# Performance work log

Measured on AMD Instinct MI355X. Metric: run time of the kernel, lower is better.

The kernel has to match this reference:

```python
import jax, jax.numpy as jnp
import numpy as np

D_MODEL = 1024
N_HEADS = 16
D_K = D_MODEL // N_HEADS
THETA = 10000.0
MAX_SEQ = 2048


def _trunc_normal(key, shape, std):
    # approximate trunc_normal in [-3std, 3std] via clipping (init only; values irrelevant to math)
    return jnp.clip(jax.random.normal(key, shape) * std, -3 * std, 3 * std).astype(jnp.float32)


def setup_inputs() -> dict:
    key = jax.random.key(0)
    kx, kq, kk, kv, ko = jax.random.split(key, 5)
    std = np.sqrt(2.0 / (D_MODEL + D_MODEL))
    x = jax.random.normal(kx, (2, 2048, D_MODEL), dtype=jnp.float32)
    W_q = _trunc_normal(kq, (D_MODEL, D_MODEL), std)
    W_k = _trunc_normal(kk, (D_MODEL, D_MODEL), std)
    W_v = _trunc_normal(kv, (D_MODEL, D_MODEL), std)
    W_o = _trunc_normal(ko, (D_MODEL, D_MODEL), std)
    return {"x": x, "W_q": W_q, "W_k": W_k, "W_v": W_v, "W_o": W_o}


def _rope(x, positions):
    # x: [b, n, s, d_k]; interleaved even/odd pairing: (x0,x1),(x2,x3),...
    d = x.shape[-1]
    inv_freq = THETA ** (-2.0 * jnp.arange(0, d // 2, dtype=jnp.float32) / d)
    angles = positions.astype(jnp.float32)[:, None] * inv_freq[None, :]  # [s, d/2]
    cos, sin = jnp.cos(angles), jnp.sin(angles)
    xp = x.reshape(x.shape[:-1] + (d // 2, 2))
    x_even, x_odd = xp[..., 0], xp[..., 1]
    out_even = x_even * cos - x_odd * sin
    out_odd = x_even * sin + x_odd * cos
    return jnp.stack((out_even, out_odd), axis=-1).reshape(x.shape)


def reference(x, W_q, W_k, W_v, W_o):
    b, s, _ = x.shape
    def split_heads(t):
        return t.reshape(b, s, N_HEADS, D_K).transpose(0, 2, 1, 3)  # b n s d
    Q = split_heads(x @ W_q.T)
    K = split_heads(x @ W_k.T)
    V = split_heads(x @ W_v.T)
    pos = jnp.arange(s)
    Q = _rope(Q, pos)
    K = _rope(K, pos)
    score = jnp.einsum('bnqd,bnkd->bnqk', Q, K) / jnp.sqrt(jnp.float32(D_K))
    causal = jnp.triu(jnp.ones((s, s), dtype=bool), k=1)
    score = jnp.where(causal[None, None], -jnp.inf, score)
    attn = jax.nn.softmax(score, axis=-1)
    out = jnp.einsum('bnqk,bnkd->bnqd', attn, V)
    out = out.transpose(0, 2, 1, 3).reshape(b, s, D_MODEL)
    return out @ W_o.T
```

## Files before the change

### kernel.cpp

```cpp
#include <hip/hip_runtime.h>

typedef float f32x4 __attribute__((ext_vector_type(4)));
typedef __bf16 bf16x8 __attribute__((ext_vector_type(8)));

#define D_MODEL 1024
#define SEQ     2048
#define NB      2
#define NH      16
#define DK      64

__device__ __forceinline__ unsigned short f2bf(float f) {
    union { float f; unsigned int u; } un; un.f = f;
    unsigned int r = un.u + 0x7fffu + ((un.u >> 16) & 1u);
    return (unsigned short)(r >> 16);
}

__device__ __forceinline__ unsigned cvtpk(float lo, float hi) {
    unsigned r;
    asm("v_cvt_pk_bf16_f32 %0, %1, %2" : "=v"(r) : "v"(lo), "v"(hi));
    return r;
}

__device__ __forceinline__ void gload16(const void* g, void* l) {
    __builtin_amdgcn_global_load_lds((__attribute__((address_space(1))) void*)g,
                                     (__attribute__((address_space(3))) void*)l,
                                     16, 0, 0);
}

__global__ __launch_bounds__(256) void cast5(
    const float* __restrict__ x,  const float* __restrict__ wq,
    const float* __restrict__ wk, const float* __restrict__ wv,
    const float* __restrict__ wo,
    unsigned short* __restrict__ xb,  unsigned short* __restrict__ wqb,
    unsigned short* __restrict__ wkb, unsigned short* __restrict__ wvb,
    unsigned short* __restrict__ wob, float2* __restrict__ tab)
{
    if (blockIdx.y == 5) {
        int idx = blockIdx.x * 256 + threadIdx.x;
        if (idx < SEQ * 32) {
            int ss = idx >> 5, p = idx & 31;
            float freq = exp2f(-0.41524101186f * (float)p);
            float sn, cs;
            sincosf((float)ss * freq, &sn, &cs);
            tab[idx] = make_float2(cs, sn);
        }
        return;
    }
    const float* src; unsigned short* dst; int n8;
    switch (blockIdx.y) {
        case 0:  src = x;  dst = xb;  n8 = (NB*SEQ*D_MODEL)/8; break;
        case 1:  src = wq; dst = wqb; n8 = (D_MODEL*D_MODEL)/8; break;
        case 2:  src = wk; dst = wkb; n8 = (D_MODEL*D_MODEL)/8; break;
        case 3:  src = wv; dst = wvb; n8 = (D_MODEL*D_MODEL)/8; break;
        default: src = wo; dst = wob; n8 = (D_MODEL*D_MODEL)/8; break;
    }
    int stride = gridDim.x * blockDim.x;
    for (int i = blockIdx.x * blockDim.x + threadIdx.x; i < n8; i += stride) {
        const float4* p = (const float4*)src + (size_t)i * 2;
        float4 a = p[0], b = p[1];
        union { unsigned short h[8]; uint4 v; } u;
        u.h[0] = f2bf(a.x); u.h[1] = f2bf(a.y); u.h[2] = f2bf(a.z); u.h[3] = f2bf(a.w);
        u.h[4] = f2bf(b.x); u.h[5] = f2bf(b.y); u.h[6] = f2bf(b.z); u.h[7] = f2bf(b.w);
        ((uint4*)dst)[i] = u.v;
    }
}

template <int MODE>
__global__ __launch_bounds__(256) void gemm_bt(
    const unsigned short* __restrict__ A,
    const unsigned short* __restrict__ B0,
    const unsigned short* __restrict__ B1,
    const unsigned short* __restrict__ B2,
    float* __restrict__ outF,
    unsigned short* __restrict__ Qh,
    unsigned short* __restrict__ Kh,
    unsigned short* __restrict__ Vt,
    const float2* __restrict__ tab,
    int M, int K)
{
    __shared__ __align__(16) unsigned short SM[3][2][128 * 32];

    const int lane = threadIdx.x & 63;
    const int wid  = threadIdx.x >> 6;
    const int l15 = lane & 15, lhi = lane >> 4;
    const int m0 = blockIdx.y * 128;
    const int n0 = blockIdx.x * 128;
    const int z  = (MODE == 1) ? (int)blockIdx.z : 0;
    const unsigned short* B = (z == 0) ? B0 : (z == 1) ? B1 : B2;
    const int waveM = (wid >> 1) * 64;
    const int waveN = (wid & 1) * 64;

    f32x4 acc[4][4];
    f32x4 zero = {0.f, 0.f, 0.f, 0.f};
#pragma unroll
    for (int m = 0; m < 4; ++m)
#pragma unroll
        for (int n = 0; n < 4; ++n) acc[m][n] = zero;

    const int lrow = lane >> 2;
    const int lcol = (lane & 3) * 8;

    auto STAGE = [&](int buf, int k0) {
#pragma unroll
        for (int q = 0; q < 2; ++q) {
            int rbase = wid * 32 + q * 16;
            gload16(A + (size_t)(m0 + rbase + lrow) * K + k0 + lcol,
                    (char*)&SM[buf][0][0] + rbase * 64);
            gload16(B + (size_t)(n0 + rbase + lrow) * K + k0 + lcol,
                    (char*)&SM[buf][1][0] + rbase * 64);
        }
    };

    const int NK = K >> 5;
    STAGE(0, 0);
    STAGE(1, 32);

    for (int k = 0; k < NK; ++k) {
        if (k < NK - 1) asm volatile("s_waitcnt vmcnt(4)" ::: "memory");
        else            asm volatile("s_waitcnt vmcnt(0)" ::: "memory");
        __builtin_amdgcn_s_barrier();
        __builtin_amdgcn_sched_barrier(0);
        if (k + 2 < NK) STAGE((k + 2) % 3, (k + 2) << 5);

        const unsigned short* as = SM[k % 3][0];
        const unsigned short* bs = SM[k % 3][1];
        bf16x8 af[4], bfr[4];
#pragma unroll
        for (int m = 0; m < 4; ++m)
            af[m] = *(const bf16x8*)(as + (waveM + m * 16 + l15) * 32 + lhi * 8);
#pragma unroll
        for (int n = 0; n < 4; ++n)
            bfr[n] = *(const bf16x8*)(bs + (waveN + n * 16 + l15) * 32 + lhi * 8);
        __builtin_amdgcn_s_setprio(1);
#pragma unroll
        for (int m = 0; m < 4; ++m)
#pragma unroll
            for (int n = 0; n < 4; ++n)
                acc[m][n] = __builtin_amdgcn_mfma_f32_16x16x32_bf16(af[m], bfr[n], acc[m][n], 0, 0, 0);
        __builtin_amdgcn_s_setprio(0);
    }

    if constexpr (MODE == 0) {
#pragma unroll
        for (int n = 0; n < 4; ++n) {
            int col = n0 + waveN + n * 16 + l15;
#pragma unroll
            for (int m = 0; m < 4; ++m) {
                int rowb = m0 + waveM + m * 16 + (lhi << 2);
#pragma unroll
                for (int r = 0; r < 4; ++r)
                    outF[(size_t)(rowb + r) * D_MODEL + col] = acc[m][n][r];
            }
        }
    } else {
        __syncthreads();
        unsigned short* Ct = ((unsigned short*)SM) + wid * 4608;
        const int colg0 = n0 + waveN;
        const int hh    = (colg0 >> 6) & (NH - 1);
        const int rowg0 = m0 + waveM;
        const int bb    = rowg0 >> 11;
        const size_t bhh = (size_t)(bb * NH + hh);

#pragma unroll
        for (int n = 0; n < 4; ++n) {
            int cl = n * 16 + l15;
#pragma unroll
            for (int m = 0; m < 4; ++m) {
#pragma unroll
                for (int r = 0; r < 4; ++r) {
                    float v  = acc[m][n][r];
                    float pv = __shfl_xor(v, 1);
                    int rl = m * 16 + (lhi << 2) + r;
                    if (z == 2) {
                        Ct[cl * 72 + rl] = f2bf(v);
                    } else {
                        int ss = (rowg0 + rl) & (SEQ - 1);
                        float2 cs = tab[(ss << 5) + (cl >> 1)];
                        float o = (cl & 1) ? (pv * cs.y + v * cs.x)
                                           : (v * cs.x - pv * cs.y);
                        if (z == 0) o *= 0.18033688011f;
                        Ct[rl * 72 + cl] = f2bf(o);
                    }
                }
            }
        }
        asm volatile("s_waitcnt lgkmcnt(0)" ::: "memory");

        const int lr = lane >> 3;
        const int lc = (lane & 7) << 3;
#pragma unroll
        for (int i = 0; i < 8; ++i) {
            int rl = i * 8 + lr;
            uint4 w = *(const uint4*)&Ct[rl * 72 + lc];
            if (z == 2) {
                int ss0 = rowg0 & (SEQ - 1);
                *(uint4*)(Vt + (bhh * DK + rl) * SEQ + ss0 + lc) = w;
            } else {
                int ss = (rowg0 + rl) & (SEQ - 1);
                unsigned short* dst = (z == 0) ? Qh : Kh;
                *(uint4*)(dst + (bhh * SEQ + ss) * DK + lc) = w;
            }
        }
    }
}

__global__ __launch_bounds__(256) void attn_kernel(
    const unsigned short* __restrict__ Qh,
    const unsigned short* __restrict__ Kh,
    const unsigned short* __restrict__ Vt,
    unsigned short* __restrict__ O)
{
    __shared__ unsigned short Ks[2][64 * 64];
    __shared__ unsigned short Vs[2][64 * 64];
    __shared__ unsigned short P[4][16 * 64];

    const int tid  = threadIdx.x;
    const int lane = tid & 63;
    const int wid  = tid >> 6;
    const int l15 = lane & 15, lhi = lane >> 4;
    const int bh = blockIdx.x;
    const int pi = blockIdx.y;
    const int b = bh >> 4, h = bh & 15;

    const unsigned short* Qb = Qh + (size_t)bh * SEQ * DK;
    const unsigned short* Kb = Kh + (size_t)bh * SEQ * DK;
    const unsigned short* Vb = Vt + (size_t)bh * DK * SEQ;

    auto STAGE = [&](int buf, int kv0s) {
#pragma unroll
        for (int c = 0; c < 2; ++c) {
            int ub = c * 256 + wid * 64;
            int u  = ub + lane;
            int kr = u >> 3;
            int kc = (u & 7) ^ (kr & 7);
            gload16(Kb + (size_t)(kv0s + kr) * DK + kc * 8, &Ks[buf][(size_t)ub * 8]);
        }
#pragma unroll
        for (int c = 0; c < 2; ++c) {
            int ub = c * 256 + wid * 64;
            int u  = ub + lane;
            int vr = u >> 3;
            int vc = (u & 7) ^ (vr & 7);
            gload16(Vb + (size_t)vr * SEQ + kv0s + vc * 8, &Vs[buf][(size_t)ub * 8]);
        }
    };

    const f32x4 zero = {0.f, 0.f, 0.f, 0.f};
    const f32x4 ninf = {-1e30f, -1e30f, -1e30f, -1e30f};

    STAGE(0, 0);
    int cur = 0;

    for (int ph = 0; ph < 2; ++ph) {
        const int qt = ph ? (31 - pi) : pi;
        const int ktl = qt;
        const int q0 = qt * 64;
        const int qw = q0 + wid * 16;

        bf16x8 qf[2];
#pragma unroll
        for (int kk = 0; kk < 2; ++kk)
            qf[kk] = *(const bf16x8*)(Qb + (size_t)(qw + l15) * DK + kk * 32 + lhi * 8);

        f32x4 oacc[4];
#pragma unroll
        for (int nd = 0; nd < 4; ++nd) oacc[nd] = zero;
        float mrow = -1e30f;
        float lrow = 0.f;

        for (int kt = 0; kt <= ktl; ++kt) {
            const int kv0 = kt << 6;
            const bool diag = (kt == ktl);
            const int nlim = diag ? (wid + 1) : 4;

            asm volatile("s_waitcnt vmcnt(0)" ::: "memory");
            __builtin_amdgcn_s_barrier();
            __builtin_amdgcn_sched_barrier(0);

            const bool hasNext = (kt < ktl) || (ph == 0);
            if (hasNext) STAGE(cur ^ 1, (kt < ktl) ? (kv0 + 64) : 0);

            f32x4 s[4];
#pragma unroll
            for (int n = 0; n < 4; ++n) s[n] = (n < nlim) ? zero : ninf;

            const int sw = l15 & 7;
            __builtin_amdgcn_s_setprio(1);
#pragma unroll
            for (int n = 0; n < 4; ++n) {
                if (n < nlim) {
                    int r = n * 16 + l15;
                    bf16x8 k0 = *(const bf16x8*)&Ks[cur][r * 64 + ((lhi ^ sw) << 3)];
                    bf16x8 k1 = *(const bf16x8*)&Ks[cur][r * 64 + (((4 + lhi) ^ sw) << 3)];
                    s[n] = __builtin_amdgcn_mfma_f32_16x16x32_bf16(k0, qf[0], s[n], 0, 0, 0);
                    s[n] = __builtin_amdgcn_mfma_f32_16x16x32_bf16(k1, qf[1], s[n], 0, 0, 0);
                }
            }
            __builtin_amdgcn_s_setprio(0);

            if (diag) {
                const int qg = qw + l15;
#pragma unroll
                for (int n = 0; n < 4; ++n) {
                    if (n < nlim) {
#pragma unroll
                        for (int r = 0; r < 4; ++r) {
                            int kg = kv0 + n * 16 + (lhi << 2) + r;
                            if (kg > qg) s[n][r] = -1e30f;
                        }
                    }
                }
            }

            float mx = fmaxf(fmaxf(s[0][0], s[0][1]), fmaxf(s[0][2], s[0][3]));
#pragma unroll
            for (int n = 1; n < 4; ++n)
                mx = fmaxf(mx, fmaxf(fmaxf(s[n][0], s[n][1]), fmaxf(s[n][2], s[n][3])));
            mx = fmaxf(mx, __shfl_xor(mx, 16));
            mx = fmaxf(mx, __shfl_xor(mx, 32));

            float alpha = 1.f;
            const int allDefer = __all(mx <= mrow + 8.f);
            if (!allDefer) {
                float mn = fmaxf(mrow, mx);
                alpha = __builtin_amdgcn_exp2f(mrow - mn);
                mrow = mn;
            }

#pragma unroll
            for (int n = 0; n < 4; ++n)
#pragma unroll
                for (int r = 0; r < 4; ++r)
                    s[n][r] = __builtin_amdgcn_exp2f(s[n][r] - mrow);

            float rs = 0.f;
#pragma unroll
            for (int n = 0; n < 4; ++n)
                rs += (s[n][0] + s[n][1]) + (s[n][2] + s[n][3]);
            rs += __shfl_xor(rs, 16);
            rs += __shfl_xor(rs, 32);
            lrow = allDefer ? (lrow + rs) : (lrow * alpha + rs);

#pragma unroll
            for (int n = 0; n < 4; ++n) {
                uint2 pk;
                pk.x = cvtpk(s[n][0], s[n][1]);
                pk.y = cvtpk(s[n][2], s[n][3]);
                int cW = 2 * n + (lhi >> 1);
                *(uint2*)&P[wid][(l15 << 6) + ((cW ^ sw) << 3) + ((lhi & 1) << 2)] = pk;
            }

            if (!allDefer) {
                float a0 = __shfl(alpha, (lhi << 2) + 0);
                float a1 = __shfl(alpha, (lhi << 2) + 1);
                float a2 = __shfl(alpha, (lhi << 2) + 2);
                float a3 = __shfl(alpha, (lhi << 2) + 3);
#pragma unroll
                for (int nd = 0; nd < 4; ++nd) {
                    oacc[nd][0] *= a0; oacc[nd][1] *= a1;
                    oacc[nd][2] *= a2; oacc[nd][3] *= a3;
                }
            }

            asm volatile("s_waitcnt lgkmcnt(0)" ::: "memory");
            const int kklim = diag ? ((nlim + 1) >> 1) : 2;
            bf16x8 pa[2];
#pragma unroll
            for (int kk = 0; kk < 2; ++kk)
                if (kk < kklim)
                    pa[kk] = *(const bf16x8*)&P[wid][(l15 << 6) + ((((kk << 2) + lhi) ^ sw) << 3)];

            __builtin_amdgcn_s_setprio(1);
#pragma unroll
            for (int nd = 0; nd < 4; ++nd)
#pragma unroll
                for (int kk = 0; kk < 2; ++kk)
                    if (kk < kklim) {
                        int rd = nd * 16 + l15;
                        bf16x8 vf = *(const bf16x8*)&Vs[cur][rd * 64 + ((((kk << 2) + lhi) ^ sw) << 3)];
                        oacc[nd] = __builtin_amdgcn_mfma_f32_16x16x32_bf16(pa[kk], vf, oacc[nd], 0, 0, 0);
                    }
            __builtin_amdgcn_s_setprio(0);

            cur ^= 1;
        }

        float inv = 1.f / lrow;
        float i0 = __shfl(inv, (lhi << 2) + 0);
        float i1 = __shfl(inv, (lhi << 2) + 1);
        float i2 = __shfl(inv, (lhi << 2) + 2);
        float i3 = __shfl(inv, (lhi << 2) + 3);
#pragma unroll
        for (int nd = 0; nd < 4; ++nd) {
            int d = nd * 16 + l15;
            int rowb = qw + (lhi << 2);
            O[((size_t)(b * SEQ + rowb + 0)) * D_MODEL + h * DK + d] = f2bf(oacc[nd][0] * i0);
            O[((size_t)(b * SEQ + rowb + 1)) * D_MODEL + h * DK + d] = f2bf(oacc[nd][1] * i1);
            O[((size_t)(b * SEQ + rowb + 2)) * D_MODEL + h * DK + d] = f2bf(oacc[nd][2] * i2);
            O[((size_t)(b * SEQ + rowb + 3)) * D_MODEL + h * DK + d] = f2bf(oacc[nd][3] * i3);
        }
    }
}

extern "C" void kernel_launch(void* const* d_in, const int* in_sizes, int n_in,
                              void* d_out, int out_size, void* d_ws, size_t ws_size,
                              hipStream_t stream)
{
    const float* x  = (const float*)d_in[0];
    const float* Wq = (const float*)d_in[1];
    const float* Wk = (const float*)d_in[2];
    const float* Wv = (const float*)d_in[3];
    const float* Wo = (const float*)d_in[4];
    float* out = (float*)d_out;

    char* ws = (char*)d_ws;
    unsigned short* xb  = (unsigned short*)(ws);
    unsigned short* Wqb = (unsigned short*)(ws + ( 8ull << 20));
    unsigned short* Wkb = (unsigned short*)(ws + (10ull << 20));
    unsigned short* Wvb = (unsigned short*)(ws + (12ull << 20));
    unsigned short* Wob = (unsigned short*)(ws + (14ull << 20));
    unsigned short* Qh  = (unsigned short*)(ws + (16ull << 20));
    unsigned short* Kh  = (unsigned short*)(ws + (24ull << 20));
    unsigned short* Vt  = (unsigned short*)(ws + (32ull << 20));
    float2*         tab = (float2*)(ws + (40ull << 20));
    unsigned short* attn = xb;

    cast5<<<dim3(512, 6), 256, 0, stream>>>(x, Wq, Wk, Wv, Wo, xb, Wqb, Wkb, Wvb, Wob, tab);

    gemm_bt<1><<<dim3(D_MODEL / 128, (NB * SEQ) / 128, 3), 256, 0, stream>>>(
        xb, Wqb, Wkb, Wvb, nullptr, Qh, Kh, Vt, tab, NB * SEQ, D_MODEL);

    attn_kernel<<<dim3(NB * NH, 16), 256, 0, stream>>>(Qh, Kh, Vt, attn);

    gemm_bt<0><<<dim3(D_MODEL / 128, (NB * SEQ) / 128, 1), 256, 0, stream>>>(
        attn, Wob, Wob, Wob, out, nullptr, nullptr, nullptr, nullptr, NB * SEQ, D_MODEL);
}
```

Measured before the change: 118.9 us.

## Remap GEMM and attention blocks for XCD locality; one q-tile per attention block

The GEMMs now launch a 1-D grid whose block index is remapped so that consecutive blocks on the same XCD share A/B tiles, and the output projection uses 64x128 tiles so it launches more blocks. The attention kernel drops the paired short/long q-tile scheme and launches one block per (head, q-tile), mapping heads to XCDs and serpentining q-tiles for load balance and L2 reuse of K/V. The aim is better L2 hit rates and occupancy. The cost is uneven per-block work in attention, which now depends on the hardware scheduler to balance it.

```diff
diff --git a/kernel.cpp b/kernel.cpp
--- a/kernel.cpp
+++ b/kernel.cpp
@@ -65,7 +65,7 @@
     }
 }
 
-template <int MODE>
+template <int MODE, int BM, int BN>
 __global__ __launch_bounds__(256) void gemm_bt(
     const unsigned short* __restrict__ A,
     const unsigned short* __restrict__ B0,
@@ -78,36 +78,53 @@
     const float2* __restrict__ tab,
     int M, int K)
 {
-    __shared__ __align__(16) unsigned short SM[3][2][128 * 32];
+    constexpr int PER_STAGE = (BM + BN) / 64;
+    constexpr int WM = BM / 2, WN = BN / 2;
+    constexpr int FM = WM / 16, FN = WN / 16;
+    __shared__ __align__(16) unsigned short SM[3 * (BM + BN) * 32];
 
     const int lane = threadIdx.x & 63;
     const int wid  = threadIdx.x >> 6;
     const int l15 = lane & 15, lhi = lane >> 4;
-    const int m0 = blockIdx.y * 128;
-    const int n0 = blockIdx.x * 128;
-    const int z  = (MODE == 1) ? (int)blockIdx.z : 0;
+
+    const int L  = blockIdx.x;
+    const int yl = L & 7;
+    const int t  = L >> 3;
+    const int bx = t & 7;
+    const int t2 = t >> 3;
+    int y, z;
+    if constexpr (MODE == 1) { y = ((t2 & 3) << 3) | yl; z = t2 >> 2; }
+    else                     { y = (t2 << 3) | yl;       z = 0;       }
+    const int m0 = y * BM;
+    const int n0 = bx * BN;
     const unsigned short* B = (z == 0) ? B0 : (z == 1) ? B1 : B2;
-    const int waveM = (wid >> 1) * 64;
-    const int waveN = (wid & 1) * 64;
-
-    f32x4 acc[4][4];
+    const int waveM = (wid >> 1) * WM;
+    const int waveN = (wid & 1) * WN;
+
+    f32x4 acc[FM][FN];
     f32x4 zero = {0.f, 0.f, 0.f, 0.f};
 #pragma unroll
-    for (int m = 0; m < 4; ++m)
-#pragma unroll
-        for (int n = 0; n < 4; ++n) acc[m][n] = zero;
+    for (int m = 0; m < FM; ++m)
+#pragma unroll
+        for (int n = 0; n < FN; ++n) acc[m][n] = zero;
 
     const int lrow = lane >> 2;
     const int lcol = (lane & 3) * 8;
 
     auto STAGE = [&](int buf, int k0) {
-#pragma unroll
-        for (int q = 0; q < 2; ++q) {
-            int rbase = wid * 32 + q * 16;
+        unsigned short* as = SM + buf * (BM + BN) * 32;
+        unsigned short* bs = as + BM * 32;
+#pragma unroll
+        for (int q = 0; q < BM / 64; ++q) {
+            int rbase = wid * (BM / 4) + q * 16;
             gload16(A + (size_t)(m0 + rbase + lrow) * K + k0 + lcol,
-                    (char*)&SM[buf][0][0] + rbase * 64);
+                    (char*)as + rbase * 64);
+        }
+#pragma unroll
+        for (int q = 0; q < BN / 64; ++q) {
+            int rbase = wid * (BN / 4) + q * 16;
             gload16(B + (size_t)(n0 + rbase + lrow) * K + k0 + lcol,
-                    (char*)&SM[buf][1][0] + rbase * 64);
+                    (char*)bs + rbase * 64);
         }
     };
 
@@ -116,36 +133,40 @@
     STAGE(1, 32);
 
     for (int k = 0; k < NK; ++k) {
-        if (k < NK - 1) asm volatile("s_waitcnt vmcnt(4)" ::: "memory");
-        else            asm volatile("s_waitcnt vmcnt(0)" ::: "memory");
+        if (k < NK - 1) {
+            if constexpr (PER_STAGE == 4) asm volatile("s_waitcnt vmcnt(4)" ::: "memory");
+            else                          asm volatile("s_waitcnt vmcnt(3)" ::: "memory");
+        } else {
+            asm volatile("s_waitcnt vmcnt(0)" ::: "memory");
+        }
         __builtin_amdgcn_s_barrier();
         __builtin_amdgcn_sched_barrier(0);
         if (k + 2 < NK) STAGE((k + 2) % 3, (k + 2) << 5);
 
-        const unsigned short* as = SM[k % 3][0];
-        const unsigned short* bs = SM[k % 3][1];
-        bf16x8 af[4], bfr[4];
-#pragma unroll
-        for (int m = 0; m < 4; ++m)
+        const unsigned short* as = SM + (k % 3) * (BM + BN) * 32;
+        const unsigned short* bs = as + BM * 32;
+        bf16x8 af[FM], bfr[FN];
+#pragma unroll
+        for (int m = 0; m < FM; ++m)
             af[m] = *(const bf16x8*)(as + (waveM + m * 16 + l15) * 32 + lhi * 8);
 #pragma unroll
-        for (int n = 0; n < 4; ++n)
+        for (int n = 0; n < FN; ++n)
             bfr[n] = *(const bf16x8*)(bs + (waveN + n * 16 + l15) * 32 + lhi * 8);
         __builtin_amdgcn_s_setprio(1);
 #pragma unroll
-        for (int m = 0; m < 4; ++m)
-#pragma unroll
-            for (int n = 0; n < 4; ++n)
+        for (int m = 0; m < FM; ++m)
+#pragma unroll
+            for (int n = 0; n < FN; ++n)
                 acc[m][n] = __builtin_amdgcn_mfma_f32_16x16x32_bf16(af[m], bfr[n], acc[m][n], 0, 0, 0);
         __builtin_amdgcn_s_setprio(0);
     }
 
     if constexpr (MODE == 0) {
 #pragma unroll
-        for (int n = 0; n < 4; ++n) {
+        for (int n = 0; n < FN; ++n) {
             int col = n0 + waveN + n * 16 + l15;
 #pragma unroll
-            for (int m = 0; m < 4; ++m) {
+            for (int m = 0; m < FM; ++m) {
                 int rowb = m0 + waveM + m * 16 + (lhi << 2);
 #pragma unroll
                 for (int r = 0; r < 4; ++r)
@@ -218,8 +239,14 @@
     const int lane = tid & 63;
     const int wid  = tid >> 6;
     const int l15 = lane & 15, lhi = lane >> 4;
-    const int bh = blockIdx.x;
-    const int pi = blockIdx.y;
+
+    const int Bk  = blockIdx.x;
+    const int xcd = Bk & 7;
+    const int r0  = Bk >> 3;
+    const int bh  = (xcd << 2) | (r0 & 3);
+    const int yq  = r0 >> 2;
+    const int g   = yq >> 3, j = yq & 7;
+    const int qt  = (g << 3) + ((g & 1) ? (7 - j) : j);
     const int b = bh >> 4, h = bh & 15;
 
     const unsigned short* Qb = Qh + (size_t)bh * SEQ * DK;
@@ -251,154 +278,149 @@
     STAGE(0, 0);
     int cur = 0;
 
-    for (int ph = 0; ph < 2; ++ph) {
-        const int qt = ph ? (31 - pi) : pi;
-        const int ktl = qt;
-        const int q0 = qt * 64;
-        const int qw = q0 + wid * 16;
-
-        bf16x8 qf[2];
-#pragma unroll
-        for (int kk = 0; kk < 2; ++kk)
-            qf[kk] = *(const bf16x8*)(Qb + (size_t)(qw + l15) * DK + kk * 32 + lhi * 8);
-
-        f32x4 oacc[4];
-#pragma unroll
-        for (int nd = 0; nd < 4; ++nd) oacc[nd] = zero;
-        float mrow = -1e30f;
-        float lrow = 0.f;
-
-        for (int kt = 0; kt <= ktl; ++kt) {
-            const int kv0 = kt << 6;
-            const bool diag = (kt == ktl);
-            const int nlim = diag ? (wid + 1) : 4;
-
-            asm volatile("s_waitcnt vmcnt(0)" ::: "memory");
-            __builtin_amdgcn_s_barrier();
-            __builtin_amdgcn_sched_barrier(0);
-
-            const bool hasNext = (kt < ktl) || (ph == 0);
-            if (hasNext) STAGE(cur ^ 1, (kt < ktl) ? (kv0 + 64) : 0);
-
-            f32x4 s[4];
-#pragma unroll
-            for (int n = 0; n < 4; ++n) s[n] = (n < nlim) ? zero : ninf;
-
-            const int sw = l15 & 7;
-            __builtin_amdgcn_s_setprio(1);
+    const int q0 = qt * 64;
+    const int qw = q0 + wid * 16;
+
+    bf16x8 qf[2];
+#pragma unroll
+    for (int kk = 0; kk < 2; ++kk)
+        qf[kk] = *(const bf16x8*)(Qb + (size_t)(qw + l15) * DK + kk * 32 + lhi * 8);
+
+    f32x4 oacc[4];
+#pragma unroll
+    for (int nd = 0; nd < 4; ++nd) oacc[nd] = zero;
+    float mrow = -1e30f;
+    float lrow = 0.f;
+
+    for (int kt = 0; kt <= qt; ++kt) {
+        const int kv0 = kt << 6;
+        const bool diag = (kt == qt);
+        const int nlim = diag ? (wid + 1) : 4;
+
+        asm volatile("s_waitcnt vmcnt(0)" ::: "memory");
+        __builtin_amdgcn_s_barrier();
+        __builtin_amdgcn_sched_barrier(0);
+
+        if (kt < qt) STAGE(cur ^ 1, kv0 + 64);
+
+        f32x4 s[4];
+#pragma unroll
+        for (int n = 0; n < 4; ++n) s[n] = (n < nlim) ? zero : ninf;
+
+        const int sw = l15 & 7;
+        __builtin_amdgcn_s_setprio(1);
+#pragma unroll
+        for (int n = 0; n < 4; ++n) {
+            if (n < nlim) {
+                int rr = n * 16 + l15;
+                bf16x8 k0 = *(const bf16x8*)&Ks[cur][rr * 64 + ((lhi ^ sw) << 3)];
+                bf16x8 k1 = *(const bf16x8*)&Ks[cur][rr * 64 + (((4 + lhi) ^ sw) << 3)];
+                s[n] = __builtin_amdgcn_mfma_f32_16x16x32_bf16(k0, qf[0], s[n], 0, 0, 0);
+                s[n] = __builtin_amdgcn_mfma_f32_16x16x32_bf16(k1, qf[1], s[n], 0, 0, 0);
+            }
+        }
+        __builtin_amdgcn_s_setprio(0);
+
+        if (diag) {
+            const int qg = qw + l15;
 #pragma unroll
             for (int n = 0; n < 4; ++n) {
                 if (n < nlim) {
-                    int r = n * 16 + l15;
-                    bf16x8 k0 = *(const bf16x8*)&Ks[cur][r * 64 + ((lhi ^ sw) << 3)];
-                    bf16x8 k1 = *(const bf16x8*)&Ks[cur][r * 64 + (((4 + lhi) ^ sw) << 3)];
-                    s[n] = __builtin_amdgcn_mfma_f32_16x16x32_bf16(k0, qf[0], s[n], 0, 0, 0);
-                    s[n] = __builtin_amdgcn_mfma_f32_16x16x32_bf16(k1, qf[1], s[n], 0, 0, 0);
-                }
-            }
-            __builtin_amdgcn_s_setprio(0);
-
-            if (diag) {
-                const int qg = qw + l15;
-#pragma unroll
-                for (int n = 0; n < 4; ++n) {
-                    if (n < nlim) {
-#pragma unroll
-                        for (int r = 0; r < 4; ++r) {
-                            int kg = kv0 + n * 16 + (lhi << 2) + r;
-                            if (kg > qg) s[n][r] = -1e30f;
-                        }
+#pragma unroll
+                    for (int rr = 0; rr < 4; ++rr) {
+                        int kg = kv0 + n * 16 + (lhi << 2) + rr;
+                        if (kg > qg) s[n][rr] = -1e30f;
                     }
                 }
             }
-
-            float mx = fmaxf(fmaxf(s[0][0], s[0][1]), fmaxf(s[0][2], s[0][3]));
-#pragma unroll
-            for (int n = 1; n < 4; ++n)
-                mx = fmaxf(mx, fmaxf(fmaxf(s[n][0], s[n][1]), fmaxf(s[n][2], s[n][3])));
-            mx = fmaxf(mx, __shfl_xor(mx, 16));
-            mx = fmaxf(mx, __shfl_xor(mx, 32));
-
-            float alpha = 1.f;
-            const int allDefer = __all(mx <= mrow + 8.f);
-            if (!allDefer) {
-                float mn = fmaxf(mrow, mx);
-                alpha = __builtin_amdgcn_exp2f(mrow - mn);
-                mrow = mn;
-            }
-
-#pragma unroll
-            for (int n = 0; n < 4; ++n)
-#pragma unroll
-                for (int r = 0; r < 4; ++r)
-                    s[n][r] = __builtin_amdgcn_exp2f(s[n][r] - mrow);
-
-            float rs = 0.f;
-#pragma unroll
-            for (int n = 0; n < 4; ++n)
-                rs += (s[n][0] + s[n][1]) + (s[n][2] + s[n][3]);
-            rs += __shfl_xor(rs, 16);
-            rs += __shfl_xor(rs, 32);
-            lrow = allDefer ? (lrow + rs) : (lrow * alpha + rs);
-
-#pragma unroll
-            for (int n = 0; n < 4; ++n) {
-                uint2 pk;
-                pk.x = cvtpk(s[n][0], s[n][1]);
-                pk.y = cvtpk(s[n][2], s[n][3]);
-                int cW = 2 * n + (lhi >> 1);
-                *(uint2*)&P[wid][(l15 << 6) + ((cW ^ sw) << 3) + ((lhi & 1) << 2)] = pk;
-            }
-
-            if (!allDefer) {
-                float a0 = __shfl(alpha, (lhi << 2) + 0);
-                float a1 = __shfl(alpha, (lhi << 2) + 1);
-                float a2 = __shfl(alpha, (lhi << 2) + 2);
-                float a3 = __shfl(alpha, (lhi << 2) + 3);
-#pragma unroll
-                for (int nd = 0; nd < 4; ++nd) {
-                    oacc[nd][0] *= a0; oacc[nd][1] *= a1;
-                    oacc[nd][2] *= a2; oacc[nd][3] *= a3;
+        }
+
+        float mx = fmaxf(fmaxf(s[0][0], s[0][1]), fmaxf(s[0][2], s[0][3]));
+#pragma unroll
+        for (int n = 1; n < 4; ++n)
+            mx = fmaxf(mx, fmaxf(fmaxf(s[n][0], s[n][1]), fmaxf(s[n][2], s[n][3])));
+        mx = fmaxf(mx, __shfl_xor(mx, 16));
+        mx = fmaxf(mx, __shfl_xor(mx, 32));
+
+        float alpha = 1.f;
+        const int allDefer = __all(mx <= mrow + 8.f);
+        if (!allDefer) {
+            float mn = fmaxf(mrow, mx);
+            alpha = __builtin_amdgcn_exp2f(mrow - mn);
+            mrow = mn;
+        }
+
+#pragma unroll
+        for (int n = 0; n < 4; ++n)
+#pragma unroll
+            for (int rr = 0; rr < 4; ++rr)
+                s[n][rr] = __builtin_amdgcn_exp2f(s[n][rr] - mrow);
+
+        float rs = 0.f;
+#pragma unroll
+        for (int n = 0; n < 4; ++n)
+            rs += (s[n][0] + s[n][1]) + (s[n][2] + s[n][3]);
+        rs += __shfl_xor(rs, 16);
+        rs += __shfl_xor(rs, 32);
+        lrow = allDefer ? (lrow + rs) : (lrow * alpha + rs);
+
+#pragma unroll
+        for (int n = 0; n < 4; ++n) {
+            uint2 pk;
+            pk.x = cvtpk(s[n][0], s[n][1]);
+            pk.y = cvtpk(s[n][2], s[n][3]);
+            int cW = 2 * n + (lhi >> 1);
+            *(uint2*)&P[wid][(l15 << 6) + ((cW ^ sw) << 3) + ((lhi & 1) << 2)] = pk;
+        }
+
+        if (!allDefer) {
+            float a0 = __shfl(alpha, (lhi << 2) + 0);
+            float a1 = __shfl(alpha, (lhi << 2) + 1);
+            float a2 = __shfl(alpha, (lhi << 2) + 2);
+            float a3 = __shfl(alpha, (lhi << 2) + 3);
+#pragma unroll
+            for (int nd = 0; nd < 4; ++nd) {
+                oacc[nd][0] *= a0; oacc[nd][1] *= a1;
+                oacc[nd][2] *= a2; oacc[nd][3] *= a3;
+            }
+        }
+
+        asm volatile("s_waitcnt lgkmcnt(0)" ::: "memory");
+        const int kklim = diag ? ((nlim + 1) >> 1) : 2;
+        bf16x8 pa[2];
+#pragma unroll
+        for (int kk = 0; kk < 2; ++kk)
+            if (kk < kklim)
+                pa[kk] = *(const bf16x8*)&P[wid][(l15 << 6) + ((((kk << 2) + lhi) ^ sw) << 3)];
+
+        __builtin_amdgcn_s_setprio(1);
+#pragma unroll
+        for (int nd = 0; nd < 4; ++nd)
+#pragma unroll
+            for (int kk = 0; kk < 2; ++kk)
+                if (kk < kklim) {
+                    int rd = nd * 16 + l15;
+                    bf16x8 vf = *(const bf16x8*)&Vs[cur][rd * 64 + ((((kk << 2) + lhi) ^ sw) << 3)];
+                    oacc[nd] = __builtin_amdgcn_mfma_f32_16x16x32_bf16(pa[kk], vf, oacc[nd], 0, 0, 0);
                 }
-            }
-
-            asm volatile("s_waitcnt lgkmcnt(0)" ::: "memory");
-            const int kklim = diag ? ((nlim + 1) >> 1) : 2;
-            bf16x8 pa[2];
-#pragma unroll
-            for (int kk = 0; kk < 2; ++kk)
-                if (kk < kklim)
-                    pa[kk] = *(const bf16x8*)&P[wid][(l15 << 6) + ((((kk << 2) + lhi) ^ sw) << 3)];
-
-            __builtin_amdgcn_s_setprio(1);
-#pragma unroll
-            for (int nd = 0; nd < 4; ++nd)
-#pragma unroll
-                for (int kk = 0; kk < 2; ++kk)
-                    if (kk < kklim) {
-                        int rd = nd * 16 + l15;
-                        bf16x8 vf = *(const bf16x8*)&Vs[cur][rd * 64 + ((((kk << 2) + lhi) ^ sw) << 3)];
-                        oacc[nd] = __builtin_amdgcn_mfma_f32_16x16x32_bf16(pa[kk], vf, oacc[nd], 0, 0, 0);
-                    }
-            __builtin_amdgcn_s_setprio(0);
-
-            cur ^= 1;
-        }
-
-        float inv = 1.f / lrow;
-        float i0 = __shfl(inv, (lhi << 2) + 0);
-        float i1 = __shfl(inv, (lhi << 2) + 1);
-        float i2 = __shfl(inv, (lhi << 2) + 2);
-        float i3 = __shfl(inv, (lhi << 2) + 3);
-#pragma unroll
-        for (int nd = 0; nd < 4; ++nd) {
-            int d = nd * 16 + l15;
-            int rowb = qw + (lhi << 2);
-            O[((size_t)(b * SEQ + rowb + 0)) * D_MODEL + h * DK + d] = f2bf(oacc[nd][0] * i0);
-            O[((size_t)(b * SEQ + rowb + 1)) * D_MODEL + h * DK + d] = f2bf(oacc[nd][1] * i1);
-            O[((size_t)(b * SEQ + rowb + 2)) * D_MODEL + h * DK + d] = f2bf(oacc[nd][2] * i2);
-            O[((size_t)(b * SEQ + rowb + 3)) * D_MODEL + h * DK + d] = f2bf(oacc[nd][3] * i3);
-        }
+        __builtin_amdgcn_s_setprio(0);
+
+        cur ^= 1;
+    }
+
+    float inv = 1.f / lrow;
+    float i0 = __shfl(inv, (lhi << 2) + 0);
+    float i1 = __shfl(inv, (lhi << 2) + 1);
+    float i2 = __shfl(inv, (lhi << 2) + 2);
+    float i3 = __shfl(inv, (lhi << 2) + 3);
+#pragma unroll
+    for (int nd = 0; nd < 4; ++nd) {
+        int d = nd * 16 + l15;
+        int rowb = qw + (lhi << 2);
+        O[((size_t)(b * SEQ + rowb + 0)) * D_MODEL + h * DK + d] = f2bf(oacc[nd][0] * i0);
+        O[((size_t)(b * SEQ + rowb + 1)) * D_MODEL + h * DK + d] = f2bf(oacc[nd][1] * i1);
+        O[((size_t)(b * SEQ + rowb + 2)) * D_MODEL + h * DK + d] = f2bf(oacc[nd][2] * i2);
+        O[((size_t)(b * SEQ + rowb + 3)) * D_MODEL + h * DK + d] = f2bf(oacc[nd][3] * i3);
     }
 }
 
@@ -427,11 +449,11 @@
 
     cast5<<<dim3(512, 6), 256, 0, stream>>>(x, Wq, Wk, Wv, Wo, xb, Wqb, Wkb, Wvb, Wob, tab);
 
-    gemm_bt<1><<<dim3(D_MODEL / 128, (NB * SEQ) / 128, 3), 256, 0, stream>>>(
+    gemm_bt<1, 128, 128><<<768, 256, 0, stream>>>(
         xb, Wqb, Wkb, Wvb, nullptr, Qh, Kh, Vt, tab, NB * SEQ, D_MODEL);
 
-    attn_kernel<<<dim3(NB * NH, 16), 256, 0, stream>>>(Qh, Kh, Vt, attn);
-
-    gemm_bt<0><<<dim3(D_MODEL / 128, (NB * SEQ) / 128, 1), 256, 0, stream>>>(
+    attn_kernel<<<1024, 256, 0, stream>>>(Qh, Kh, Vt, attn);
+
+    gemm_bt<0, 64, 128><<<512, 256, 0, stream>>>(
         attn, Wob, Wob, Wob, out, nullptr, nullptr, nullptr, nullptr, NB * SEQ, D_MODEL);
 }
```

After: 116.7 us. Within noise of the previous version (-1.8%).
